# Kernel tuning notes

Hardware: AMD Instinct MI355X
Metric: run time of the kernel (lower is better)

Reference implementation:

```python
import jax, jax.numpy as jnp
import numpy as np

_OFFS = np.array([(dx, dy, dz) for dx in (-1, 0, 1) for dy in (-1, 0, 1) for dz in (-1, 0, 1)], np.int64)


def setup_inputs() -> dict:
    rng = np.random.default_rng(0)
    B, G, NPTS = 2, 128, 100000
    # level-0 active voxel coords (batch, x, y, z)
    cs = []
    for b in range(B):
        xyz = np.unique(rng.integers(0, G, size=(NPTS, 3)), axis=0)
        cs.append(np.concatenate([np.full((len(xyz), 1), b, np.int64), xyz], 1))
    c0 = np.concatenate(cs, 0)
    c1 = np.unique(np.concatenate([c0[:, :1], c0[:, 1:] // 2], 1), axis=0)  # stride-2 coords
    c2 = np.unique(np.concatenate([c1[:, :1], c1[:, 1:] // 2], 1), axis=0)  # stride-4 coords

    def table(c, g):  # dense coordinate hash: coord -> row index, -1 if empty
        t = np.full((B, g, g, g), -1, np.int64)
        t[c[:, 0], c[:, 1], c[:, 2], c[:, 3]] = np.arange(len(c))
        return t

    t0, t1, t2 = table(c0, G), table(c1, G // 2), table(c2, G // 4)

    def kmap(out_c, tab, g, stride):  # kernel map for k=3 conv: [27, Nout], -1 = no neighbor
        base = out_c[:, 1:] * stride
        nbr = np.empty((27, len(out_c)), np.int32)
        for k, off in enumerate(_OFFS):
            p = base + off
            ok = ((p >= 0) & (p < g)).all(1)
            pc = np.clip(p, 0, g - 1)
            nbr[k] = np.where(ok, tab[out_c[:, 0], pc[:, 0], pc[:, 1], pc[:, 2]], -1)
        return nbr

    nbr0 = kmap(c0, t0, G, 1)        # enc1: submanifold, out coords == in coords
    nbr1 = kmap(c1, t0, G, 2)        # enc2: stride-2 downsample
    nbr2 = kmap(c2, t1, G // 2, 2)   # enc3: stride-2 downsample

    def upmap(fine_c, coarse_tab):   # k=2 s=2 transposed conv: unique parent + offset id
        q = fine_c[:, 1:] // 2
        idx = coarse_tab[fine_c[:, 0], q[:, 0], q[:, 1], q[:, 2]].astype(np.int32)
        r = fine_c[:, 1:] - 2 * q
        off = (r[:, 0] * 4 + r[:, 1] * 2 + r[:, 2]).astype(np.int32)
        return idx, off

    up1_idx, up1_off = upmap(c1, t2)  # dec2: level2 -> level1
    up0_idx, up0_off = upmap(c0, t1)  # dec1: level1 -> level0

    def w(shape):
        return jnp.asarray(rng.normal(0.0, 0.05, shape).astype(np.float32))

    feats = jnp.asarray(rng.normal(0.0, 1.0, (len(c0), 2)).astype(np.float32))
    return dict(
        feats=feats,
        W1=w((27, 2, 32)), W2=w((27, 32, 64)), W3=w((27, 64, 128)),
        W4=w((8, 128, 64)), W5=w((8, 64, 32)), Wout=w((32, 2)),
        g1=jnp.ones(32), b1=jnp.zeros(32), g2=jnp.ones(64), b2=jnp.zeros(64),
        g3=jnp.ones(128), b3=jnp.zeros(128), g4=jnp.ones(64), b4=jnp.zeros(64),
        g5=jnp.ones(32), b5=jnp.zeros(32),
        nbr0=jnp.asarray(nbr0), nbr1=jnp.asarray(nbr1), nbr2=jnp.asarray(nbr2),
        up1_idx=jnp.asarray(up1_idx), up1_off=jnp.asarray(up1_off),
        up0_idx=jnp.asarray(up0_idx), up0_off=jnp.asarray(up0_off),
    )


def _sconv(f, nbr, W):
    # implicit-GEMM sparse conv: gather per kernel offset, matmul, masked accumulate
    out = jnp.zeros((nbr.shape[1], W.shape[2]), f.dtype)
    for k in range(W.shape[0]):
        idx = nbr[k]
        g = jnp.where((idx >= 0)[:, None], f[jnp.maximum(idx, 0)], 0.0)
        out = out + g @ W[k]
    return out


def _upconv(f, pidx, poff, W):
    # k=2 s=2 transposed conv: each fine voxel has exactly one coarse parent + offset id in [0,8)
    g = f[pidx]
    out = jnp.zeros((g.shape[0], W.shape[2]), f.dtype)
    for k in range(8):
        out = out + jnp.where((poff == k)[:, None], g @ W[k], 0.0)
    return out


def _bn_relu(x, g, b):
    # training-mode BatchNorm over the voxel dim (biased var), then ReLU
    mu = x.mean(0)
    var = x.var(0)
    return jax.nn.relu((x - mu) * jax.lax.rsqrt(var + 1e-5) * g + b)


def reference(feats, W1, W2, W3, W4, W5, Wout, g1, b1, g2, b2, g3, b3, g4, b4, g5, b5,
              nbr0, nbr1, nbr2, up1_idx, up1_off, up0_idx, up0_off):
    e1 = _bn_relu(_sconv(feats, nbr0, W1), g1, b1)   # [N0, 32]
    e2 = _bn_relu(_sconv(e1, nbr1, W2), g2, b2)      # [N1, 64]
    e3 = _bn_relu(_sconv(e2, nbr2, W3), g3, b3)      # [N2, 128]
    d2 = _bn_relu(_upconv(e3, up1_idx, up1_off, W4), g4, b4)  # [N1, 64]
    d1 = _bn_relu(_upconv(d2, up0_idx, up0_off, W5), g5, b5)  # [N0, 32]
    return d1 @ Wout                                  # 1x1 conv, [N0, 2]
```

## Files before the change

kernel.cpp:

```cpp
#include <hip/hip_runtime.h>
#include <hip/hip_bf16.h>

typedef __attribute__((ext_vector_type(4))) float  f32x4;
typedef __attribute__((ext_vector_type(8))) short  short8;
typedef __attribute__((ext_vector_type(2))) float  flt2;
typedef long long ll;

__device__ __forceinline__ short f2bf(float f) {
    __hip_bfloat16 h = __float2bfloat16(f);
    short s; __builtin_memcpy(&s, &h, 2);
    return s;
}
__device__ __forceinline__ float bf2f(short s) {
    unsigned u = ((unsigned)(unsigned short)s) << 16;
    float f; __builtin_memcpy(&f, &u, 4);
    return f;
}
__device__ __forceinline__ void gload_lds16(const void* g, void* l) {
    __builtin_amdgcn_global_load_lds(
        (const __attribute__((address_space(1))) unsigned*)(g),
        (__attribute__((address_space(3))) unsigned*)(l),
        16, 0, 0);
}
__device__ __forceinline__ int xcd_swz(int bid, int nwg) {
    int q8 = nwg >> 3, r8 = nwg & 7;
    int xcd = bid & 7, j = bid >> 3;
    return (xcd < r8 ? xcd * (q8 + 1) : r8 * (q8 + 1) + (xcd - r8) * q8) + j;
}

__global__ void prep_kernel(const float* __restrict__ W1, const float* __restrict__ W2,
                            const float* __restrict__ W3, const float* __restrict__ W4,
                            const float* __restrict__ W5,
                            short* W1t, short* W2t, short* W3t, short* W4t, short* W5t) {
    int gid = blockIdx.x * 256 + threadIdx.x;
    if (gid < 32 * 64) {
        int co = gid >> 6, e = gid & 63;
        float v = 0.f;
        if (e < 54) { int k = e >> 1, ci = e & 1; v = W1[(k * 2 + ci) * 32 + co]; }
        W1t[gid] = f2bf(v);
        return;
    }
    int g = gid - 32 * 64;
    if (g < 28 * 2048) { int k = g / 2048, r = g % 2048, co = r >> 5, ci = r & 31;
        W2t[g] = (k < 27) ? f2bf(W2[((ll)k * 32 + ci) * 64 + co]) : (short)0; return; }
    g -= 28 * 2048;
    if (g < 28 * 8192) { int k = g / 8192, r = g % 8192, co = r >> 6, ci = r & 63;
        W3t[g] = (k < 27) ? f2bf(W3[((ll)k * 64 + ci) * 128 + co]) : (short)0; return; }
    g -= 28 * 8192;
    if (g < 8 * 64 * 128) { int k = g / (64*128), r = g % (64*128), co = r >> 7, ci = r & 127;
        W4t[g] = f2bf(W4[((ll)k * 128 + ci) * 64 + co]); return; }
    g -= 8 * 64 * 128;
    if (g < 8 * 32 * 64) { int k = g / (32*64), r = g % (32*64), co = r >> 6, ci = r & 63;
        W5t[g] = f2bf(W5[((ll)k * 64 + ci) * 32 + co]); return; }
}

__launch_bounds__(256)
__global__ void c1_kernel(const float* __restrict__ feats, const int* __restrict__ nbr,
                          const short* __restrict__ W1t, short* __restrict__ out,
                          float* __restrict__ part, int N) {
    __shared__ float sc[8 * 32];
    const int wgid = xcd_swz(blockIdx.x, gridDim.x);
    int tid = threadIdx.x, lane = tid & 63, wave = tid >> 6;
    int rb = wgid * 64 + wave * 16;
    int r = rb + (lane & 15);
    int rl = r < N ? r : N - 1;
    int seg = lane >> 4, l15 = lane & 15;
    f32x4 acc[2];
    acc[0] = (f32x4){0,0,0,0}; acc[1] = (f32x4){0,0,0,0};
    short8 a[2];
    #pragma unroll
    for (int kc = 0; kc < 2; ++kc) {
        #pragma unroll
        for (int j = 0; j < 4; ++j) {
            int k = kc * 16 + seg * 4 + j;
            flt2 f = (flt2){0.f, 0.f};
            if (k < 27) {
                int idx = nbr[(ll)k * N + rl];
                if (idx >= 0) f = *(const flt2*)(feats + 2 * (ll)idx);
            }
            a[kc][2*j]   = f2bf(f[0]);
            a[kc][2*j+1] = f2bf(f[1]);
        }
    }
    #pragma unroll
    for (int kc = 0; kc < 2; ++kc)
        #pragma unroll
        for (int c = 0; c < 2; ++c) {
            short8 b = *(const short8*)(W1t + (c*16 + l15) * 64 + kc * 32 + seg * 8);
            acc[c] = __builtin_amdgcn_mfma_f32_16x16x32_bf16(a[kc], b, acc[c], 0, 0, 0);
        }
    int r0 = rb + seg * 4;
    #pragma unroll
    for (int c = 0; c < 2; ++c) {
        int col = c * 16 + l15;
        #pragma unroll
        for (int j = 0; j < 4; ++j)
            if (r0 + j < N) out[(ll)(r0 + j) * 32 + col] = f2bf(acc[c][j]);
    }
    float s[2], q[2];
    #pragma unroll
    for (int c = 0; c < 2; ++c) { s[c] = 0.f; q[c] = 0.f; }
    #pragma unroll
    for (int c = 0; c < 2; ++c)
        #pragma unroll
        for (int j = 0; j < 4; ++j) {
            float v = (r0 + j < N) ? acc[c][j] : 0.f;
            s[c] += v; q[c] += v * v;
        }
    #pragma unroll
    for (int c = 0; c < 2; ++c) {
        s[c] += __shfl_xor(s[c], 16); q[c] += __shfl_xor(q[c], 16);
        s[c] += __shfl_xor(s[c], 32); q[c] += __shfl_xor(q[c], 32);
    }
    if (lane < 16) {
        #pragma unroll
        for (int c = 0; c < 2; ++c) {
            sc[(wave * 2 + 0) * 32 + c * 16 + l15] = s[c];
            sc[(wave * 2 + 1) * 32 + c * 16 + l15] = q[c];
        }
    }
    __syncthreads();
    for (int i = tid; i < 32; i += 256) {
        float ss = sc[0*32+i] + sc[2*32+i] + sc[4*32+i] + sc[6*32+i];
        float qq = sc[1*32+i] + sc[3*32+i] + sc[5*32+i] + sc[7*32+i];
        part[(ll)wgid * 64 + i]      = ss;
        part[(ll)wgid * 64 + 32 + i] = qq;
    }
}

template<int CIN, int COLS, int RG, int MINW>
__launch_bounds__(256, MINW)
__global__ void msconv7_kernel(const short* __restrict__ inb, const int* __restrict__ nbr,
                               const short* __restrict__ Wt, short* __restrict__ out,
                               float* __restrict__ part, int N, int zoff) {
    constexpr int KC = CIN / 32, NT = COLS / 16;
    constexpr int CPK = COLS * CIN / 8, BIT = CPK / 256;
    constexpr int WST = COLS * CIN;
    constexpr int SH = (CIN == 32) ? 6 : 7;
    __shared__ __align__(16) short lb[2][WST];

    const int wgid = xcd_swz(blockIdx.x, gridDim.x);
    const int tid = threadIdx.x, lane = tid & 63, wave = tid >> 6;
    const int seg = lane >> 4, l15 = lane & 15;
    const int wrb = wgid * (64 * RG) + wave * (16 * RG);
    const char* inB = (const char*)inb;

    int rl[RG];
    #pragma unroll
    for (int rg = 0; rg < RG; ++rg) {
        int r = wrb + rg * 16 + l15;
        rl[rg] = r < N ? r : N - 1;
    }

    auto rawIdx = [&](int k, int (&ix)[RG]) {
        #pragma unroll
        for (int rg = 0; rg < RG; ++rg) ix[rg] = nbr[(ll)k * N + rl[rg]];
    };
    auto mkoff = [&](const int (&ix)[RG], int (&o)[RG]) {
        #pragma unroll
        for (int rg = 0; rg < RG; ++rg) o[rg] = (ix[rg] >= 0) ? (ix[rg] << SH) : zoff;
    };
    auto stage = [&](int kn, int buf) {
        #pragma unroll
        for (int it = 0; it < BIT; ++it) {
            int q = it * 256 + tid;
            int co = q % COLS, sg = (q / COLS) & 3, kc = q / (COLS * 4);
            gload_lds16(Wt + (ll)kn * WST + co * CIN + kc * 32 + sg * 8, &lb[buf][q * 8]);
        }
    };
    auto ldA = [&](short8 (&a)[RG][KC], const int (&o)[RG]) {
        #pragma unroll
        for (int rg = 0; rg < RG; ++rg) {
            const char* base = inB + o[rg];
            #pragma unroll
            for (int kc = 0; kc < KC; ++kc)
                a[rg][kc] = *(const short8*)(base + kc * 64 + seg * 16);
        }
    };

    f32x4 acc[RG][NT];
    #pragma unroll
    for (int rg = 0; rg < RG; ++rg)
        #pragma unroll
        for (int c = 0; c < NT; ++c) acc[rg][c] = (f32x4){0.f, 0.f, 0.f, 0.f};

    auto compute = [&](int buf, short8 (&a)[RG][KC]) {
        #pragma unroll
        for (int kc = 0; kc < KC; ++kc)
            #pragma unroll
            for (int c = 0; c < NT; ++c) {
                short8 b = *(const short8*)&lb[buf][((kc * 4 + seg) * COLS + c * 16 + l15) * 8];
                #pragma unroll
                for (int rg = 0; rg < RG; ++rg)
                    acc[rg][c] = __builtin_amdgcn_mfma_f32_16x16x32_bf16(
                        a[rg][kc], b, acc[rg][c], 0, 0, 0);
            }
    };

    short8 aA[RG][KC], aB[RG][KC];
    int iF[RG], offC[RG];

    {
        int i0[RG], i1[RG], o0[RG];
        rawIdx(0, i0); rawIdx(1, i1); rawIdx(2, iF);
        mkoff(i0, o0); mkoff(i1, offC);
        stage(0, 0);
        __builtin_amdgcn_sched_barrier(0);
        ldA(aA, o0);
        __builtin_amdgcn_sched_barrier(0);
        asm volatile("s_waitcnt vmcnt(%0) lgkmcnt(0)" :: "n"(RG * KC) : "memory");
        __builtin_amdgcn_s_barrier();
        __builtin_amdgcn_sched_barrier(0);
    }

    #pragma unroll
    for (int k = 0; k < 27; ++k) {
        int iN[RG];
        if (k + 1 < 27) {
            if (k + 3 < 27) rawIdx(k + 3, iN);
            __builtin_amdgcn_sched_barrier(0);
            stage(k + 1, (k + 1) & 1);
            __builtin_amdgcn_sched_barrier(0);
            if (k & 1) ldA(aA, offC); else ldA(aB, offC);
            __builtin_amdgcn_sched_barrier(0);
        }
        if (k & 1) compute(1, aB); else compute(0, aA);
        if (k + 1 < 27) {
            __builtin_amdgcn_sched_barrier(0);
            asm volatile("s_waitcnt vmcnt(%0) lgkmcnt(0)" :: "n"(RG * KC) : "memory");
            __builtin_amdgcn_s_barrier();
            __builtin_amdgcn_sched_barrier(0);
            mkoff(iF, offC);
            if (k + 3 < 27) {
                #pragma unroll
                for (int rg = 0; rg < RG; ++rg) iF[rg] = iN[rg];
            }
        }
    }

    #pragma unroll
    for (int rg = 0; rg < RG; ++rg)
        #pragma unroll
        for (int c = 0; c < NT; ++c) {
            int col = c * 16 + l15;
            #pragma unroll
            for (int j = 0; j < 4; ++j) {
                int rr = wrb + rg * 16 + seg * 4 + j;
                if (rr < N) out[(ll)rr * COLS + col] = f2bf(acc[rg][c][j]);
            }
        }

    float s[NT], q[NT];
    #pragma unroll
    for (int c = 0; c < NT; ++c) { s[c] = 0.f; q[c] = 0.f; }
    #pragma unroll
    for (int rg = 0; rg < RG; ++rg)
        #pragma unroll
        for (int c = 0; c < NT; ++c)
            #pragma unroll
            for (int j = 0; j < 4; ++j) {
                int rr = wrb + rg * 16 + seg * 4 + j;
                float v = (rr < N) ? acc[rg][c][j] : 0.f;
                s[c] += v; q[c] += v * v;
            }
    #pragma unroll
    for (int c = 0; c < NT; ++c) {
        s[c] += __shfl_xor(s[c], 16); q[c] += __shfl_xor(q[c], 16);
        s[c] += __shfl_xor(s[c], 32); q[c] += __shfl_xor(q[c], 32);
    }
    __syncthreads();
    float* sc = (float*)&lb[0][0];
    if (lane < 16) {
        #pragma unroll
        for (int c = 0; c < NT; ++c) {
            sc[(wave * 2 + 0) * COLS + c * 16 + l15] = s[c];
            sc[(wave * 2 + 1) * COLS + c * 16 + l15] = q[c];
        }
    }
    __syncthreads();
    for (int i = tid; i < COLS; i += 256) {
        float ss = sc[0*COLS+i] + sc[2*COLS+i] + sc[4*COLS+i] + sc[6*COLS+i];
        float qq = sc[1*COLS+i] + sc[3*COLS+i] + sc[5*COLS+i] + sc[7*COLS+i];
        part[(ll)wgid * 2 * COLS + i]        = ss;
        part[(ll)wgid * 2 * COLS + COLS + i] = qq;
    }
}

__global__ void dcountB_kernel(const int* __restrict__ poffA, int NA, int* __restrict__ cntA,
                               const int* __restrict__ poffB, int NB, int* __restrict__ cntB) {
    const int* poff = blockIdx.y ? poffB : poffA;
    int* cnt = blockIdx.y ? cntB : cntA;
    int N = blockIdx.y ? NB : NA;
    __shared__ int lc[8];
    if (threadIdx.x < 8) lc[threadIdx.x] = 0;
    __syncthreads();
    int r = blockIdx.x * 256 + threadIdx.x;
    if (r < N) atomicAdd(&lc[poff[r]], 1);
    __syncthreads();
    if (threadIdx.x < 8 && lc[threadIdx.x]) atomicAdd(&cnt[threadIdx.x], lc[threadIdx.x]);
}

__global__ void dprefixB_kernel(const int* __restrict__ cntA, int* basesA, int* kofbA,
                                int* permA, int nblkA,
                                const int* __restrict__ cntB, int* basesB, int* kofbB,
                                int* permB, int nblkB) {
    const int* cnt = blockIdx.x ? cntB : cntA;
    int* bases = blockIdx.x ? basesB : basesA;
    int* kofb  = blockIdx.x ? kofbB  : kofbA;
    int* perm  = blockIdx.x ? permB  : permA;
    int nblk   = blockIdx.x ? nblkB  : nblkA;
    __shared__ int base[9];
    if (threadIdx.x == 0) {
        int b = 0;
        for (int k = 0; k < 8; ++k) { base[k] = b; b += (cnt[k] + 63) & ~63; }
        base[8] = b;
        for (int k = 0; k < 9; ++k) bases[k] = base[k];
    }
    __syncthreads();
    int nb = base[8] >> 6;
    for (int i = threadIdx.x; i < nblk; i += 256) {
        int k = -1;
        if (i < nb) {
            int rb = i << 6; k = 0;
            while (rb >= base[k + 1]) ++k;
        }
        kofb[i] = k;
    }
    for (int k = 0; k < 8; ++k) {
        int s = base[k] + cnt[k], e = base[k + 1];
        for (int i = s + threadIdx.x; i < e; i += 256) perm[i] = -1;
    }
}

__global__ void dscatterB_kernel(const int* __restrict__ poffA, const int* basesA,
                                 int* curA, int* permA, int NA,
                                 const int* __restrict__ poffB, const int* basesB,
                                 int* curB, int* permB, int NB) {
    const int* poff = blockIdx.y ? poffB : poffA;
    const int* bases = blockIdx.y ? basesB : basesA;
    int* curp = blockIdx.y ? curB : curA;
    int* perm = blockIdx.y ? permB : permA;
    int N = blockIdx.y ? NB : NA;
    __shared__ int lc[8], lbs[8];
    if (threadIdx.x < 8) lc[threadIdx.x] = 0;
    __syncthreads();
    int r = blockIdx.x * 256 + threadIdx.x;
    int k = 0, myl = 0;
    if (r < N) { k = poff[r]; myl = atomicAdd(&lc[k], 1); }
    __syncthreads();
    if (threadIdx.x < 8) lbs[threadIdx.x] = atomicAdd(&curp[threadIdx.x], lc[threadIdx.x]);
    __syncthreads();
    if (r < N) perm[bases[k] + lbs[k] + myl] = r;
}

template<int CIN, int COUT>
__launch_bounds__(256)
__global__ void gdec_kernel(const short* __restrict__ inb, const int* __restrict__ perm,
                            const int* __restrict__ kofb, const int* __restrict__ pidx,
                            const short* __restrict__ Wt, const short* __restrict__ zrow,
                            short* __restrict__ out, float* __restrict__ part) {
    constexpr int KC = CIN / 32, NT = COUT / 16;
    constexpr int CPK = COUT * CIN / 8, BIT = CPK / 256;
    __shared__ __align__(16) short lb[COUT * CIN];
    const int wgid = xcd_swz(blockIdx.x, gridDim.x);
    const int tid = threadIdx.x, lane = tid & 63, wave = tid >> 6;
    int k = kofb[wgid];
    if (k < 0) {
        for (int i = tid; i < 2 * COUT; i += 256) part[(ll)wgid * 2 * COUT + i] = 0.f;
        return;
    }
    const int seg = lane >> 4, l15 = lane & 15;
    const int wrb = wgid * 64 + wave * 16;
    int rl = wrb + l15;
    int pr = perm[rl];
    int idx = pr < 0 ? -1 : pidx[pr];

    #pragma unroll
    for (int it = 0; it < BIT; ++it) {
        int q = it * 256 + tid;
        int co = q % COUT, sg = (q / COUT) & 3, kc = q / (COUT * 4);
        gload_lds16(Wt + ((ll)k * COUT + co) * CIN + kc * 32 + sg * 8, &lb[q * 8]);
    }
    short8 a[KC];
    const short* base = (idx < 0) ? zrow : (inb + (ll)idx * CIN);
    #pragma unroll
    for (int kc = 0; kc < KC; ++kc)
        a[kc] = *(const short8*)(base + kc * 32 + seg * 8);

    f32x4 acc[NT];
    #pragma unroll
    for (int c = 0; c < NT; ++c) acc[c] = (f32x4){0.f, 0.f, 0.f, 0.f};
    __syncthreads();
    #pragma unroll
    for (int kc = 0; kc < KC; ++kc)
        #pragma unroll
        for (int c = 0; c < NT; ++c) {
            short8 b = *(const short8*)&lb[((kc * 4 + seg) * COUT + c * 16 + l15) * 8];
            acc[c] = __builtin_amdgcn_mfma_f32_16x16x32_bf16(a[kc], b, acc[c], 0, 0, 0);
        }
    #pragma unroll
    for (int j = 0; j < 4; ++j) {
        int prs = __shfl(pr, seg * 4 + j, 64);
        if (prs >= 0) {
            #pragma unroll
            for (int c = 0; c < NT; ++c)
                out[(ll)prs * COUT + c * 16 + l15] = f2bf(acc[c][j]);
        }
    }
    float s[NT], q[NT];
    #pragma unroll
    for (int c = 0; c < NT; ++c) { s[c] = 0.f; q[c] = 0.f; }
    #pragma unroll
    for (int c = 0; c < NT; ++c)
        #pragma unroll
        for (int j = 0; j < 4; ++j) { float v = acc[c][j]; s[c] += v; q[c] += v * v; }
    #pragma unroll
    for (int c = 0; c < NT; ++c) {
        s[c] += __shfl_xor(s[c], 16); q[c] += __shfl_xor(q[c], 16);
        s[c] += __shfl_xor(s[c], 32); q[c] += __shfl_xor(q[c], 32);
    }
    __syncthreads();
    float* sc = (float*)lb;
    if (lane < 16) {
        #pragma unroll
        for (int c = 0; c < NT; ++c) {
            sc[(wave * 2 + 0) * COUT + c * 16 + l15] = s[c];
            sc[(wave * 2 + 1) * COUT + c * 16 + l15] = q[c];
        }
    }
    __syncthreads();
    for (int i = tid; i < COUT; i += 256) {
        float ss = sc[0*COUT+i] + sc[2*COUT+i] + sc[4*COUT+i] + sc[6*COUT+i];
        float qq = sc[1*COUT+i] + sc[3*COUT+i] + sc[5*COUT+i] + sc[7*COUT+i];
        part[(ll)wgid * 2 * COUT + i]        = ss;
        part[(ll)wgid * 2 * COUT + COUT + i] = qq;
    }
}

__global__ void red2_kernel(const float* __restrict__ part, int nblk,
                            const float* __restrict__ g, const float* __restrict__ bb,
                            float* __restrict__ A, float* __restrict__ B, int C, int N) {
    int c = blockIdx.x;
    float s = 0.f, q = 0.f;
    for (int i = threadIdx.x; i < nblk; i += 256) {
        s += part[(ll)i * 2 * C + c];
        q += part[(ll)i * 2 * C + C + c];
    }
    __shared__ float ls[256], lq[256];
    ls[threadIdx.x] = s; lq[threadIdx.x] = q;
    __syncthreads();
    for (int str = 128; str >= 1; str >>= 1) {
        if (threadIdx.x < str) {
            ls[threadIdx.x] += ls[threadIdx.x + str];
            lq[threadIdx.x] += lq[threadIdx.x + str];
        }
        __syncthreads();
    }
    if (threadIdx.x == 0) {
        float inv = 1.0f / (float)N;
        float mu = ls[0] * inv, var = lq[0] * inv - mu * mu;
        float a = g[c] * rsqrtf(var + 1e-5f);
        A[c] = a; B[c] = bb[c] - mu * a;
    }
}

template<int C>
__global__ void bnrelu_kernel(const short* __restrict__ x, const float* __restrict__ A,
                              const float* __restrict__ B, short* __restrict__ out, int N) {
    constexpr int CPR = C / 8;
    int i = blockIdx.x * 256 + threadIdx.x;
    if (i >= N * CPR) return;
    int r = i / CPR, ch = i - r * CPR;
    short8 v = *(const short8*)(x + (ll)r * C + ch * 8);
    short8 o;
    #pragma unroll
    for (int j = 0; j < 8; ++j) {
        int c = ch * 8 + j;
        float y = fmaf(bf2f(v[j]), A[c], B[c]);
        o[j] = f2bf(y > 0.f ? y : 0.f);
    }
    *(short8*)(out + (ll)r * C + ch * 8) = o;
}

__global__ void outk_kernel(const short* __restrict__ z, const float* __restrict__ A,
                            const float* __restrict__ B, const float* __restrict__ Wout,
                            float* __restrict__ out, int N) {
    __shared__ float w[64], sa[32], sb[32];
    if (threadIdx.x < 64) w[threadIdx.x] = Wout[threadIdx.x];
    if (threadIdx.x < 32) { sa[threadIdx.x] = A[threadIdx.x]; sb[threadIdx.x] = B[threadIdx.x]; }
    __syncthreads();
    int r = blockIdx.x * 256 + threadIdx.x;
    if (r >= N) return;
    const short* zp = z + (ll)r * 32;
    float o0 = 0.f, o1 = 0.f;
    #pragma unroll
    for (int s4 = 0; s4 < 4; ++s4) {
        short8 v = *(const short8*)(zp + s4 * 8);
        #pragma unroll
        for (int j = 0; j < 8; ++j) {
            int c = s4 * 8 + j;
            float y = fmaf(bf2f(v[j]), sa[c], sb[c]);
            y = y > 0.f ? y : 0.f;
            o0 = fmaf(y, w[2*c], o0);
            o1 = fmaf(y, w[2*c+1], o1);
        }
    }
    out[(ll)r * 2]     = o0;
    out[(ll)r * 2 + 1] = o1;
}

extern "C" void kernel_launch(void* const* d_in, const int* in_sizes, int n_in,
                              void* d_out, int out_size, void* d_ws, size_t ws_size,
                              hipStream_t stream) {
    const float* feats = (const float*)d_in[0];
    const float* W1 = (const float*)d_in[1];
    const float* W2 = (const float*)d_in[2];
    const float* W3 = (const float*)d_in[3];
    const float* W4 = (const float*)d_in[4];
    const float* W5 = (const float*)d_in[5];
    const float* Wout = (const float*)d_in[6];
    const float* g1 = (const float*)d_in[7],  *b1 = (const float*)d_in[8];
    const float* g2 = (const float*)d_in[9],  *b2 = (const float*)d_in[10];
    const float* g3 = (const float*)d_in[11], *b3 = (const float*)d_in[12];
    const float* g4 = (const float*)d_in[13], *b4 = (const float*)d_in[14];
    const float* g5 = (const float*)d_in[15], *b5 = (const float*)d_in[16];
    const int* nbr0 = (const int*)d_in[17];
    const int* nbr1 = (const int*)d_in[18];
    const int* nbr2 = (const int*)d_in[19];
    const int* up1_idx = (const int*)d_in[20];
    const int* up1_off = (const int*)d_in[21];
    const int* up0_idx = (const int*)d_in[22];
    const int* up0_off = (const int*)d_in[23];

    const int N0 = in_sizes[0] / 2;
    const int N1 = in_sizes[20];
    const int N2 = in_sizes[19] / 27;

    char* cur = (char*)d_ws;
    auto alloc = [&](size_t bytes) { char* p = cur; cur += (bytes + 255) & ~255ULL; return p; };
    auto cdiv = [](ll a, ll b) { return (int)((a + b - 1) / b); };

    float* stats = (float*)alloc(4096);
    float* A1 = stats,       *B1c = stats + 32;
    float* A2 = stats + 64,  *B2c = stats + 128;
    float* A3 = stats + 192, *B3c = stats + 320;
    float* A4 = stats + 448, *B4c = stats + 512;
    float* A5 = stats + 576, *B5c = stats + 608;
    short* zrow  = (short*)((char*)stats + 2560);
    int*   cnt4  = (int*)((char*)stats + 3072);
    int*   cur4  = (int*)((char*)stats + 3104);
    int*   cnt5  = (int*)((char*)stats + 3136);
    int*   cur5  = (int*)((char*)stats + 3168);
    int*   bas4  = (int*)((char*)stats + 3200);
    int*   bas5  = (int*)((char*)stats + 3264);

    float* part = (float*)alloc(2 * 1024 * 1024);

    size_t zmax = (size_t)N1 * 64;
    if ((size_t)N0 * 32  > zmax) zmax = (size_t)N0 * 32;
    if ((size_t)N2 * 128 > zmax) zmax = (size_t)N2 * 128;
    short* zb  = (short*)alloc(zmax * 2);
    short* e1b = (short*)alloc((size_t)N0 * 32 * 2);
    short* e2b = (short*)alloc((size_t)N1 * 64 * 2);
    short* e3b = (short*)alloc((size_t)N2 * 128 * 2);
    short* d2b = (short*)alloc((size_t)N1 * 64 * 2);
    short* W1t = (short*)alloc(32 * 64 * 2);
    short* W2t = (short*)alloc((size_t)28 * 64 * 32 * 2);
    short* W3t = (short*)alloc((size_t)28 * 128 * 64 * 2);
    short* W4t = (short*)alloc((size_t)8 * 64 * 128 * 2);
    short* W5t = (short*)alloc((size_t)8 * 32 * 64 * 2);

    const int gridL4 = cdiv((ll)N1 + 512, 64);
    const int gridL5 = cdiv((ll)N0 + 512, 64);
    int* perm4 = (int*)alloc((size_t)gridL4 * 64 * 4);
    int* kofb4 = (int*)alloc((size_t)gridL4 * 4);
    int* perm5 = (int*)alloc((size_t)gridL5 * 64 * 4);
    int* kofb5 = (int*)alloc((size_t)gridL5 * 4);

    const int zoff1 = (int)((ll)((char*)zrow - (char*)e1b));
    const int zoff2 = (int)((ll)((char*)zrow - (char*)e2b));

    const int nblk1 = cdiv(N0, 64);
    const int nblk2 = cdiv(N1, 128);
    const int nblk3 = cdiv(N2, 128);

    hipMemsetAsync((char*)stats + 2560, 0, 640, stream);

    prep_kernel<<<cdiv(2048 + 28*2048 + 28*8192 + 65536 + 16384, 256), 256, 0, stream>>>(
        W1, W2, W3, W4, W5, W1t, W2t, W3t, W4t, W5t);

    {
        int gx = cdiv(N1 > N0 ? N1 : N0, 256);
        dcountB_kernel<<<dim3(gx, 2), 256, 0, stream>>>(up1_off, N1, cnt4, up0_off, N0, cnt5);
        dprefixB_kernel<<<2, 256, 0, stream>>>(cnt4, bas4, kofb4, perm4, gridL4,
                                               cnt5, bas5, kofb5, perm5, gridL5);
        dscatterB_kernel<<<dim3(gx, 2), 256, 0, stream>>>(up1_off, bas4, cur4, perm4, N1,
                                                          up0_off, bas5, cur5, perm5, N0);
    }

    c1_kernel<<<nblk1, 256, 0, stream>>>(feats, nbr0, W1t, zb, part, N0);
    red2_kernel<<<32, 256, 0, stream>>>(part, nblk1, g1, b1, A1, B1c, 32, N0);
    bnrelu_kernel<32><<<cdiv((ll)N0 * 4, 256), 256, 0, stream>>>(zb, A1, B1c, e1b, N0);

    msconv7_kernel<32, 64, 2, 4><<<nblk2, 256, 0, stream>>>(e1b, nbr1, W2t, zb, part, N1, zoff1);
    red2_kernel<<<64, 256, 0, stream>>>(part, nblk2, g2, b2, A2, B2c, 64, N1);
    bnrelu_kernel<64><<<cdiv((ll)N1 * 8, 256), 256, 0, stream>>>(zb, A2, B2c, e2b, N1);

    msconv7_kernel<64, 128, 2, 3><<<nblk3, 256, 0, stream>>>(e2b, nbr2, W3t, zb, part, N2, zoff2);
    red2_kernel<<<128, 256, 0, stream>>>(part, nblk3, g3, b3, A3, B3c, 128, N2);
    bnrelu_kernel<128><<<cdiv((ll)N2 * 16, 256), 256, 0, stream>>>(zb, A3, B3c, e3b, N2);

    gdec_kernel<128, 64><<<gridL4, 256, 0, stream>>>(e3b, perm4, kofb4, up1_idx, W4t, zrow, zb, part);
    red2_kernel<<<64, 256, 0, stream>>>(part, gridL4, g4, b4, A4, B4c, 64, N1);
    bnrelu_kernel<64><<<cdiv((ll)N1 * 8, 256), 256, 0, stream>>>(zb, A4, B4c, d2b, N1);

    gdec_kernel<64, 32><<<gridL5, 256, 0, stream>>>(d2b, perm5, kofb5, up0_idx, W5t, zrow, zb, part);
    red2_kernel<<<32, 256, 0, stream>>>(part, gridL5, g5, b5, A5, B5c, 32, N0);
    outk_kernel<<<cdiv(N0, 256), 256, 0, stream>>>(zb, A5, B5c, Wout, (float*)d_out, N0);
}
```

Measured before the change: 240.8 us.

## Fuse BatchNorm+ReLU into consumer conv gathers, drop standalone bnrelu kernels

Removes the separate bnrelu kernels between stages. Each conv and decoder kernel now loads the raw pre-BN bf16 activations, applies the per-channel scale/shift and ReLU in registers, and masks invalid neighbors to zero instead of pointing them at a zero row. This saves four kernel launches and one full write and read of each intermediate tensor. The cost is recomputing the BN transform for every gathered neighbor (27 times per input row in the sparse convs). It also changes occupancy and row-group settings: MINW drops from 4 to 3 for enc2, and enc3 goes to RG=1 with 64-row blocks.

```diff
diff --git a/kernel.cpp b/kernel.cpp
--- a/kernel.cpp
+++ b/kernel.cpp
@@ -130,9 +130,10 @@
 
 template<int CIN, int COLS, int RG, int MINW>
 __launch_bounds__(256, MINW)
-__global__ void msconv7_kernel(const short* __restrict__ inb, const int* __restrict__ nbr,
-                               const short* __restrict__ Wt, short* __restrict__ out,
-                               float* __restrict__ part, int N, int zoff) {
+__global__ void msconv8_kernel(const short* __restrict__ inb, const int* __restrict__ nbr,
+                               const short* __restrict__ Wt,
+                               const float* __restrict__ Abn, const float* __restrict__ Bbn,
+                               short* __restrict__ out, float* __restrict__ part, int N) {
     constexpr int KC = CIN / 32, NT = COLS / 16;
     constexpr int CPK = COLS * CIN / 8, BIT = CPK / 256;
     constexpr int WST = COLS * CIN;
@@ -156,9 +157,12 @@
         #pragma unroll
         for (int rg = 0; rg < RG; ++rg) ix[rg] = nbr[(ll)k * N + rl[rg]];
     };
-    auto mkoff = [&](const int (&ix)[RG], int (&o)[RG]) {
-        #pragma unroll
-        for (int rg = 0; rg < RG; ++rg) o[rg] = (ix[rg] >= 0) ? (ix[rg] << SH) : zoff;
+    auto mkoff = [&](const int (&ix)[RG], int (&o)[RG], int (&v)[RG]) {
+        #pragma unroll
+        for (int rg = 0; rg < RG; ++rg) {
+            v[rg] = (ix[rg] >= 0);
+            o[rg] = (ix[rg] >= 0 ? ix[rg] : 0) << SH;
+        }
     };
     auto stage = [&](int kn, int buf) {
         #pragma unroll
@@ -178,13 +182,34 @@
         }
     };
 
+    f32x4 cA[KC][2], cB[KC][2];
+    #pragma unroll
+    for (int kc = 0; kc < KC; ++kc) {
+        cA[kc][0] = *(const f32x4*)(Abn + kc * 32 + seg * 8);
+        cA[kc][1] = *(const f32x4*)(Abn + kc * 32 + seg * 8 + 4);
+        cB[kc][0] = *(const f32x4*)(Bbn + kc * 32 + seg * 8);
+        cB[kc][1] = *(const f32x4*)(Bbn + kc * 32 + seg * 8 + 4);
+    }
+
     f32x4 acc[RG][NT];
     #pragma unroll
     for (int rg = 0; rg < RG; ++rg)
         #pragma unroll
         for (int c = 0; c < NT; ++c) acc[rg][c] = (f32x4){0.f, 0.f, 0.f, 0.f};
 
-    auto compute = [&](int buf, short8 (&a)[RG][KC]) {
+    auto compute = [&](int buf, short8 (&a)[RG][KC], const int (&v)[RG]) {
+        short8 t[RG][KC];
+        #pragma unroll
+        for (int rg = 0; rg < RG; ++rg)
+            #pragma unroll
+            for (int kc = 0; kc < KC; ++kc)
+                #pragma unroll
+                for (int j = 0; j < 8; ++j) {
+                    float x = bf2f(a[rg][kc][j]);
+                    float y = fmaf(x, cA[kc][j >> 2][j & 3], cB[kc][j >> 2][j & 3]);
+                    y = y > 0.f ? y : 0.f;
+                    t[rg][kc][j] = v[rg] ? f2bf(y) : (short)0;
+                }
         #pragma unroll
         for (int kc = 0; kc < KC; ++kc)
             #pragma unroll
@@ -193,20 +218,22 @@
                 #pragma unroll
                 for (int rg = 0; rg < RG; ++rg)
                     acc[rg][c] = __builtin_amdgcn_mfma_f32_16x16x32_bf16(
-                        a[rg][kc], b, acc[rg][c], 0, 0, 0);
+                        t[rg][kc], b, acc[rg][c], 0, 0, 0);
             }
     };
 
     short8 aA[RG][KC], aB[RG][KC];
-    int iF[RG], offC[RG];
+    int iF[RG], offC[RG], vldC[RG], vA[RG], vB[RG];
 
     {
-        int i0[RG], i1[RG], o0[RG];
+        int i0[RG], i1[RG], o0[RG], v0[RG];
         rawIdx(0, i0); rawIdx(1, i1); rawIdx(2, iF);
-        mkoff(i0, o0); mkoff(i1, offC);
+        mkoff(i0, o0, v0); mkoff(i1, offC, vldC);
         stage(0, 0);
         __builtin_amdgcn_sched_barrier(0);
         ldA(aA, o0);
+        #pragma unroll
+        for (int rg = 0; rg < RG; ++rg) vA[rg] = v0[rg];
         __builtin_amdgcn_sched_barrier(0);
         asm volatile("s_waitcnt vmcnt(%0) lgkmcnt(0)" :: "n"(RG * KC) : "memory");
         __builtin_amdgcn_s_barrier();
@@ -221,16 +248,24 @@
             __builtin_amdgcn_sched_barrier(0);
             stage(k + 1, (k + 1) & 1);
             __builtin_amdgcn_sched_barrier(0);
-            if (k & 1) ldA(aA, offC); else ldA(aB, offC);
+            if (k & 1) {
+                ldA(aA, offC);
+                #pragma unroll
+                for (int rg = 0; rg < RG; ++rg) vA[rg] = vldC[rg];
+            } else {
+                ldA(aB, offC);
+                #pragma unroll
+                for (int rg = 0; rg < RG; ++rg) vB[rg] = vldC[rg];
+            }
             __builtin_amdgcn_sched_barrier(0);
         }
-        if (k & 1) compute(1, aB); else compute(0, aA);
+        if (k & 1) compute(1, aB, vB); else compute(0, aA, vA);
         if (k + 1 < 27) {
             __builtin_amdgcn_sched_barrier(0);
             asm volatile("s_waitcnt vmcnt(%0) lgkmcnt(0)" :: "n"(RG * KC) : "memory");
             __builtin_amdgcn_s_barrier();
             __builtin_amdgcn_sched_barrier(0);
-            mkoff(iF, offC);
+            mkoff(iF, offC, vldC);
             if (k + 3 < 27) {
                 #pragma unroll
                 for (int rg = 0; rg < RG; ++rg) iF[rg] = iN[rg];
@@ -357,7 +392,8 @@
 __launch_bounds__(256)
 __global__ void gdec_kernel(const short* __restrict__ inb, const int* __restrict__ perm,
                             const int* __restrict__ kofb, const int* __restrict__ pidx,
-                            const short* __restrict__ Wt, const short* __restrict__ zrow,
+                            const short* __restrict__ Wt,
+                            const float* __restrict__ Abn, const float* __restrict__ Bbn,
                             short* __restrict__ out, float* __restrict__ part) {
     constexpr int KC = CIN / 32, NT = COUT / 16;
     constexpr int CPK = COUT * CIN / 8, BIT = CPK / 256;
@@ -374,6 +410,7 @@
     int rl = wrb + l15;
     int pr = perm[rl];
     int idx = pr < 0 ? -1 : pidx[pr];
+    int valid = (idx >= 0);
 
     #pragma unroll
     for (int it = 0; it < BIT; ++it) {
@@ -381,11 +418,27 @@
         int co = q % COUT, sg = (q / COUT) & 3, kc = q / (COUT * 4);
         gload_lds16(Wt + ((ll)k * COUT + co) * CIN + kc * 32 + sg * 8, &lb[q * 8]);
     }
+    f32x4 cA[KC][2], cB[KC][2];
+    #pragma unroll
+    for (int kc = 0; kc < KC; ++kc) {
+        cA[kc][0] = *(const f32x4*)(Abn + kc * 32 + seg * 8);
+        cA[kc][1] = *(const f32x4*)(Abn + kc * 32 + seg * 8 + 4);
+        cB[kc][0] = *(const f32x4*)(Bbn + kc * 32 + seg * 8);
+        cB[kc][1] = *(const f32x4*)(Bbn + kc * 32 + seg * 8 + 4);
+    }
     short8 a[KC];
-    const short* base = (idx < 0) ? zrow : (inb + (ll)idx * CIN);
-    #pragma unroll
-    for (int kc = 0; kc < KC; ++kc)
-        a[kc] = *(const short8*)(base + kc * 32 + seg * 8);
+    const short* base = inb + (ll)(idx < 0 ? 0 : idx) * CIN;
+    #pragma unroll
+    for (int kc = 0; kc < KC; ++kc) {
+        short8 raw = *(const short8*)(base + kc * 32 + seg * 8);
+        #pragma unroll
+        for (int j = 0; j < 8; ++j) {
+            float x = bf2f(raw[j]);
+            float y = fmaf(x, cA[kc][j >> 2][j & 3], cB[kc][j >> 2][j & 3]);
+            y = y > 0.f ? y : 0.f;
+            a[kc][j] = valid ? f2bf(y) : (short)0;
+        }
+    }
 
     f32x4 acc[NT];
     #pragma unroll
@@ -462,24 +515,6 @@
         float a = g[c] * rsqrtf(var + 1e-5f);
         A[c] = a; B[c] = bb[c] - mu * a;
     }
-}
-
-template<int C>
-__global__ void bnrelu_kernel(const short* __restrict__ x, const float* __restrict__ A,
-                              const float* __restrict__ B, short* __restrict__ out, int N) {
-    constexpr int CPR = C / 8;
-    int i = blockIdx.x * 256 + threadIdx.x;
-    if (i >= N * CPR) return;
-    int r = i / CPR, ch = i - r * CPR;
-    short8 v = *(const short8*)(x + (ll)r * C + ch * 8);
-    short8 o;
-    #pragma unroll
-    for (int j = 0; j < 8; ++j) {
-        int c = ch * 8 + j;
-        float y = fmaf(bf2f(v[j]), A[c], B[c]);
-        o[j] = f2bf(y > 0.f ? y : 0.f);
-    }
-    *(short8*)(out + (ll)r * C + ch * 8) = o;
 }
 
 __global__ void outk_kernel(const short* __restrict__ z, const float* __restrict__ A,
@@ -546,7 +581,6 @@
     float* A3 = stats + 192, *B3c = stats + 320;
     float* A4 = stats + 448, *B4c = stats + 512;
     float* A5 = stats + 576, *B5c = stats + 608;
-    short* zrow  = (short*)((char*)stats + 2560);
     int*   cnt4  = (int*)((char*)stats + 3072);
     int*   cur4  = (int*)((char*)stats + 3104);
     int*   cnt5  = (int*)((char*)stats + 3136);
@@ -556,14 +590,11 @@
 
     float* part = (float*)alloc(2 * 1024 * 1024);
 
-    size_t zmax = (size_t)N1 * 64;
-    if ((size_t)N0 * 32  > zmax) zmax = (size_t)N0 * 32;
-    if ((size_t)N2 * 128 > zmax) zmax = (size_t)N2 * 128;
-    short* zb  = (short*)alloc(zmax * 2);
-    short* e1b = (short*)alloc((size_t)N0 * 32 * 2);
-    short* e2b = (short*)alloc((size_t)N1 * 64 * 2);
-    short* e3b = (short*)alloc((size_t)N2 * 128 * 2);
-    short* d2b = (short*)alloc((size_t)N1 * 64 * 2);
+    short* z1 = (short*)alloc((size_t)N0 * 32 * 2);
+    short* z2 = (short*)alloc((size_t)N1 * 64 * 2);
+    short* z3 = (short*)alloc((size_t)N2 * 128 * 2);
+    short* z4 = (short*)alloc((size_t)N1 * 64 * 2);
+    short* z5 = (short*)alloc((size_t)N0 * 32 * 2);
     short* W1t = (short*)alloc(32 * 64 * 2);
     short* W2t = (short*)alloc((size_t)28 * 64 * 32 * 2);
     short* W3t = (short*)alloc((size_t)28 * 128 * 64 * 2);
@@ -577,14 +608,11 @@
     int* perm5 = (int*)alloc((size_t)gridL5 * 64 * 4);
     int* kofb5 = (int*)alloc((size_t)gridL5 * 4);
 
-    const int zoff1 = (int)((ll)((char*)zrow - (char*)e1b));
-    const int zoff2 = (int)((ll)((char*)zrow - (char*)e2b));
-
     const int nblk1 = cdiv(N0, 64);
     const int nblk2 = cdiv(N1, 128);
-    const int nblk3 = cdiv(N2, 128);
-
-    hipMemsetAsync((char*)stats + 2560, 0, 640, stream);
+    const int nblk3 = cdiv(N2, 64);
+
+    hipMemsetAsync((char*)stats + 3072, 0, 128, stream);
 
     prep_kernel<<<cdiv(2048 + 28*2048 + 28*8192 + 65536 + 16384, 256), 256, 0, stream>>>(
         W1, W2, W3, W4, W5, W1t, W2t, W3t, W4t, W5t);
@@ -598,23 +626,20 @@
                                                           up0_off, bas5, cur5, perm5, N0);
     }
 
-    c1_kernel<<<nblk1, 256, 0, stream>>>(feats, nbr0, W1t, zb, part, N0);
+    c1_kernel<<<nblk1, 256, 0, stream>>>(feats, nbr0, W1t, z1, part, N0);
     red2_kernel<<<32, 256, 0, stream>>>(part, nblk1, g1, b1, A1, B1c, 32, N0);
-    bnrelu_kernel<32><<<cdiv((ll)N0 * 4, 256), 256, 0, stream>>>(zb, A1, B1c, e1b, N0);
-
-    msconv7_kernel<32, 64, 2, 4><<<nblk2, 256, 0, stream>>>(e1b, nbr1, W2t, zb, part, N1, zoff1);
+
+    msconv8_kernel<32, 64, 2, 3><<<nblk2, 256, 0, stream>>>(z1, nbr1, W2t, A1, B1c, z2, part, N1);
     red2_kernel<<<64, 256, 0, stream>>>(part, nblk2, g2, b2, A2, B2c, 64, N1);
-    bnrelu_kernel<64><<<cdiv((ll)N1 * 8, 256), 256, 0, stream>>>(zb, A2, B2c, e2b, N1);
-
-    msconv7_kernel<64, 128, 2, 3><<<nblk3, 256, 0, stream>>>(e2b, nbr2, W3t, zb, part, N2, zoff2);
+
+    msconv8_kernel<64, 128, 1, 3><<<nblk3, 256, 0, stream>>>(z2, nbr2, W3t, A2, B2c, z3, part, N2);
     red2_kernel<<<128, 256, 0, stream>>>(part, nblk3, g3, b3, A3, B3c, 128, N2);
-    bnrelu_kernel<128><<<cdiv((ll)N2 * 16, 256), 256, 0, stream>>>(zb, A3, B3c, e3b, N2);
-
-    gdec_kernel<128, 64><<<gridL4, 256, 0, stream>>>(e3b, perm4, kofb4, up1_idx, W4t, zrow, zb, part);
+
+    gdec_kernel<128, 64><<<gridL4, 256, 0, stream>>>(z3, perm4, kofb4, up1_idx, W4t, A3, B3c, z4, part);
     red2_kernel<<<64, 256, 0, stream>>>(part, gridL4, g4, b4, A4, B4c, 64, N1);
-    bnrelu_kernel<64><<<cdiv((ll)N1 * 8, 256), 256, 0, stream>>>(zb, A4, B4c, d2b, N1);
-
-    gdec_kernel<64, 32><<<gridL5, 256, 0, stream>>>(d2b, perm5, kofb5, up0_idx, W5t, zrow, zb, part);
+
+    gdec_kernel<64, 32><<<gridL5, 256, 0, stream>>>(z4, perm5, kofb5, up0_idx, W5t, A4, B4c, z5, part);
     red2_kernel<<<32, 256, 0, stream>>>(part, gridL5, g5, b5, A5, B5c, 32, N0);
-    outk_kernel<<<cdiv(N0, 256), 256, 0, stream>>>(zb, A5, B5c, Wout, (float*)d_out, N0);
-}
+
+    outk_kernel<<<cdiv(N0, 256), 256, 0, stream>>>(z5, A5, B5c, Wout, (float*)d_out, N0);
+}
```

Measured after the change: 257.9 us. 7.1% more time.

## Fuse BN+ReLU into decoder gather loads and retile level-3 conv

Applied to the files above, without the earlier changes.

The decoder kernels now apply the previous layer's batch-norm affine and ReLU while gathering parent rows, so the separate bnrelu passes before each upconv are removed. Each stage gets its own pre-activation buffer instead of sharing one scratch buffer, because raw conv outputs must stay live for the later fused consumer. The level-3 sparse conv also switches to a smaller rows-per-block tiling with more blocks. This saves two full read/write passes over the activations. In exchange, every gathered element is normalised again per fine voxel, and memory use rises.

```diff
diff --git a/kernel.cpp b/kernel.cpp
--- a/kernel.cpp
+++ b/kernel.cpp
@@ -357,7 +357,8 @@
 __launch_bounds__(256)
 __global__ void gdec_kernel(const short* __restrict__ inb, const int* __restrict__ perm,
                             const int* __restrict__ kofb, const int* __restrict__ pidx,
-                            const short* __restrict__ Wt, const short* __restrict__ zrow,
+                            const short* __restrict__ Wt,
+                            const float* __restrict__ Abn, const float* __restrict__ Bbn,
                             short* __restrict__ out, float* __restrict__ part) {
     constexpr int KC = CIN / 32, NT = COUT / 16;
     constexpr int CPK = COUT * CIN / 8, BIT = CPK / 256;
@@ -374,6 +375,7 @@
     int rl = wrb + l15;
     int pr = perm[rl];
     int idx = pr < 0 ? -1 : pidx[pr];
+    int valid = (idx >= 0);
 
     #pragma unroll
     for (int it = 0; it < BIT; ++it) {
@@ -381,11 +383,27 @@
         int co = q % COUT, sg = (q / COUT) & 3, kc = q / (COUT * 4);
         gload_lds16(Wt + ((ll)k * COUT + co) * CIN + kc * 32 + sg * 8, &lb[q * 8]);
     }
+    f32x4 cA[KC][2], cB[KC][2];
+    #pragma unroll
+    for (int kc = 0; kc < KC; ++kc) {
+        cA[kc][0] = *(const f32x4*)(Abn + kc * 32 + seg * 8);
+        cA[kc][1] = *(const f32x4*)(Abn + kc * 32 + seg * 8 + 4);
+        cB[kc][0] = *(const f32x4*)(Bbn + kc * 32 + seg * 8);
+        cB[kc][1] = *(const f32x4*)(Bbn + kc * 32 + seg * 8 + 4);
+    }
     short8 a[KC];
-    const short* base = (idx < 0) ? zrow : (inb + (ll)idx * CIN);
-    #pragma unroll
-    for (int kc = 0; kc < KC; ++kc)
-        a[kc] = *(const short8*)(base + kc * 32 + seg * 8);
+    const short* base = inb + (ll)(idx < 0 ? 0 : idx) * CIN;
+    #pragma unroll
+    for (int kc = 0; kc < KC; ++kc) {
+        short8 raw = *(const short8*)(base + kc * 32 + seg * 8);
+        #pragma unroll
+        for (int j = 0; j < 8; ++j) {
+            float x = bf2f(raw[j]);
+            float y = fmaf(x, cA[kc][j >> 2][j & 3], cB[kc][j >> 2][j & 3]);
+            y = y > 0.f ? y : 0.f;
+            a[kc][j] = valid ? f2bf(y) : (short)0;
+        }
+    }
 
     f32x4 acc[NT];
     #pragma unroll
@@ -556,14 +574,13 @@
 
     float* part = (float*)alloc(2 * 1024 * 1024);
 
-    size_t zmax = (size_t)N1 * 64;
-    if ((size_t)N0 * 32  > zmax) zmax = (size_t)N0 * 32;
-    if ((size_t)N2 * 128 > zmax) zmax = (size_t)N2 * 128;
-    short* zb  = (short*)alloc(zmax * 2);
+    short* z1  = (short*)alloc((size_t)N0 * 32 * 2);
     short* e1b = (short*)alloc((size_t)N0 * 32 * 2);
+    short* z2  = (short*)alloc((size_t)N1 * 64 * 2);
     short* e2b = (short*)alloc((size_t)N1 * 64 * 2);
-    short* e3b = (short*)alloc((size_t)N2 * 128 * 2);
-    short* d2b = (short*)alloc((size_t)N1 * 64 * 2);
+    short* z3  = (short*)alloc((size_t)N2 * 128 * 2);
+    short* z4  = (short*)alloc((size_t)N1 * 64 * 2);
+    short* z5  = (short*)alloc((size_t)N0 * 32 * 2);
     short* W1t = (short*)alloc(32 * 64 * 2);
     short* W2t = (short*)alloc((size_t)28 * 64 * 32 * 2);
     short* W3t = (short*)alloc((size_t)28 * 128 * 64 * 2);
@@ -582,7 +599,7 @@
 
     const int nblk1 = cdiv(N0, 64);
     const int nblk2 = cdiv(N1, 128);
-    const int nblk3 = cdiv(N2, 128);
+    const int nblk3 = cdiv(N2, 64);
 
     hipMemsetAsync((char*)stats + 2560, 0, 640, stream);
 
@@ -598,23 +615,22 @@
                                                           up0_off, bas5, cur5, perm5, N0);
     }
 
-    c1_kernel<<<nblk1, 256, 0, stream>>>(feats, nbr0, W1t, zb, part, N0);
+    c1_kernel<<<nblk1, 256, 0, stream>>>(feats, nbr0, W1t, z1, part, N0);
     red2_kernel<<<32, 256, 0, stream>>>(part, nblk1, g1, b1, A1, B1c, 32, N0);
-    bnrelu_kernel<32><<<cdiv((ll)N0 * 4, 256), 256, 0, stream>>>(zb, A1, B1c, e1b, N0);
-
-    msconv7_kernel<32, 64, 2, 4><<<nblk2, 256, 0, stream>>>(e1b, nbr1, W2t, zb, part, N1, zoff1);
+    bnrelu_kernel<32><<<cdiv((ll)N0 * 4, 256), 256, 0, stream>>>(z1, A1, B1c, e1b, N0);
+
+    msconv7_kernel<32, 64, 2, 4><<<nblk2, 256, 0, stream>>>(e1b, nbr1, W2t, z2, part, N1, zoff1);
     red2_kernel<<<64, 256, 0, stream>>>(part, nblk2, g2, b2, A2, B2c, 64, N1);
-    bnrelu_kernel<64><<<cdiv((ll)N1 * 8, 256), 256, 0, stream>>>(zb, A2, B2c, e2b, N1);
-
-    msconv7_kernel<64, 128, 2, 3><<<nblk3, 256, 0, stream>>>(e2b, nbr2, W3t, zb, part, N2, zoff2);
+    bnrelu_kernel<64><<<cdiv((ll)N1 * 8, 256), 256, 0, stream>>>(z2, A2, B2c, e2b, N1);
+
+    msconv7_kernel<64, 128, 1, 3><<<nblk3, 256, 0, stream>>>(e2b, nbr2, W3t, z3, part, N2, zoff2);
     red2_kernel<<<128, 256, 0, stream>>>(part, nblk3, g3, b3, A3, B3c, 128, N2);
-    bnrelu_kernel<128><<<cdiv((ll)N2 * 16, 256), 256, 0, stream>>>(zb, A3, B3c, e3b, N2);
-
-    gdec_kernel<128, 64><<<gridL4, 256, 0, stream>>>(e3b, perm4, kofb4, up1_idx, W4t, zrow, zb, part);
+
+    gdec_kernel<128, 64><<<gridL4, 256, 0, stream>>>(z3, perm4, kofb4, up1_idx, W4t, A3, B3c, z4, part);
     red2_kernel<<<64, 256, 0, stream>>>(part, gridL4, g4, b4, A4, B4c, 64, N1);
-    bnrelu_kernel<64><<<cdiv((ll)N1 * 8, 256), 256, 0, stream>>>(zb, A4, B4c, d2b, N1);
-
-    gdec_kernel<64, 32><<<gridL5, 256, 0, stream>>>(d2b, perm5, kofb5, up0_idx, W5t, zrow, zb, part);
+
+    gdec_kernel<64, 32><<<gridL5, 256, 0, stream>>>(z4, perm5, kofb5, up0_idx, W5t, A4, B4c, z5, part);
     red2_kernel<<<32, 256, 0, stream>>>(part, gridL5, g5, b5, A5, B5c, 32, N0);
-    outk_kernel<<<cdiv(N0, 256), 256, 0, stream>>>(zb, A5, B5c, Wout, (float*)d_out, N0);
-}
+
+    outk_kernel<<<cdiv(N0, 256), 256, 0, stream>>>(z5, A5, B5c, Wout, (float*)d_out, N0);
+}
```

Result: slower. 256.6 us (+6.6%).
